# Optimization experiments

Measured on AMD Instinct MI355X. Metric: run time of the kernel, lower is better.

The kernel has to match this reference:

```python
import jax, jax.numpy as jnp
import numpy as np

NUM_HEADS = 16
MODEL_DIM = 1024
DEPTH = MODEL_DIM // NUM_HEADS
B, S = 4, 1024


def setup_inputs() -> dict:
    key = jax.random.key(0)
    ks = jax.random.split(key, 12)
    sc = 1.0 / np.sqrt(MODEL_DIM)
    q = jax.random.normal(ks[0], (B, S, MODEL_DIM), jnp.float32)
    k = jax.random.normal(ks[1], (B, S, MODEL_DIM), jnp.float32)
    v = jax.random.normal(ks[2], (B, S, MODEL_DIM), jnp.float32)
    # binary padding mask, 1 = masked position (added as mask * -1e9)
    mask = (jax.random.uniform(ks[3], (B, 1, 1, S)) < 0.1).astype(jnp.float32)
    Wq = jax.random.normal(ks[4], (MODEL_DIM, MODEL_DIM), jnp.float32) * sc
    bq = jnp.zeros((MODEL_DIM,), jnp.float32)
    Wk = jax.random.normal(ks[5], (MODEL_DIM, MODEL_DIM), jnp.float32) * sc
    bk = jnp.zeros((MODEL_DIM,), jnp.float32)
    Wv = jax.random.normal(ks[6], (MODEL_DIM, MODEL_DIM), jnp.float32) * sc
    bv = jnp.zeros((MODEL_DIM,), jnp.float32)
    Wo = jax.random.normal(ks[7], (MODEL_DIM, MODEL_DIM), jnp.float32) * sc
    bo = jnp.zeros((MODEL_DIM,), jnp.float32)
    return dict(q=q, k=k, v=v, mask=mask, Wq=Wq, bq=bq, Wk=Wk, bk=bk,
                Wv=Wv, bv=bv, Wo=Wo, bo=bo)


def _split_head(x):
    b, s, _ = x.shape
    return x.reshape(b, s, NUM_HEADS, DEPTH).transpose(0, 2, 1, 3)


def reference(q, k, v, mask, Wq, bq, Wk, bk, Wv, bv, Wo, bo):
    Q = _split_head(q @ Wq + bq)   # (B,H,S,depth)
    K = _split_head(k @ Wk + bk)
    V = _split_head(v @ Wv + bv)
    # NOTE: original divides by k_dim (depth), NOT sqrt(depth) -- keep faithful
    logits = jnp.einsum('bhqd,bhkd->bhqk', Q, K) / jnp.float32(DEPTH)
    logits = logits + mask * (-1e9)
    attn = jax.nn.softmax(logits, axis=-1)         # (B,H,Sq,Sk)
    ctx = jnp.einsum('bhqk,bhkd->bhqd', attn, V)   # (B,H,S,depth)
    ctx = ctx.transpose(0, 2, 1, 3).reshape(q.shape[0], -1, MODEL_DIM)
    out = ctx @ Wo + bo
    return out, attn
```

## Files before the change

### kernel.cpp

```cpp
#include <hip/hip_runtime.h>
#include <stdint.h>
#include <stddef.h>

#define DEV __device__ __forceinline__

typedef __bf16 bf16_t;
typedef bf16_t bf16x8 __attribute__((ext_vector_type(8)));
typedef float f32x4 __attribute__((ext_vector_type(4)));
typedef unsigned short us4 __attribute__((ext_vector_type(4)));
typedef unsigned short us8 __attribute__((ext_vector_type(8)));

DEV float bf2f(unsigned short u) {
    union { unsigned int i; float f; } w; w.i = ((unsigned int)u) << 16; return w.f;
}
DEV unsigned short f2bf(float f) {
    union { unsigned int i; float f; } w; w.f = f;
    unsigned int u = w.i;
    return (unsigned short)((u + 0x7fffu + ((u >> 16) & 1u)) >> 16);
}

DEV void gl_lds16(const void* g, void* l) {
    __builtin_amdgcn_global_load_lds((const __attribute__((address_space(1))) void*)g,
                                     (__attribute__((address_space(3))) void*)l,
                                     16, 0, 0);
}

__global__ void __launch_bounds__(256)
cvt_f32_bf16(const float* __restrict__ src, unsigned short* __restrict__ dst) {
    int idx = (blockIdx.x * 256 + threadIdx.x) * 4;
    f32x4 v = *(const f32x4*)&src[idx];
    us4 o;
#pragma unroll
    for (int i = 0; i < 4; i++) o[i] = f2bf(v[i]);
    *(us4*)&dst[idx] = o;
}

__global__ void __launch_bounds__(256)
transpose_w(const float* __restrict__ W0, const float* __restrict__ W1,
            const float* __restrict__ W2, const float* __restrict__ W3,
            unsigned short* __restrict__ T0, unsigned short* __restrict__ T1,
            unsigned short* __restrict__ T2, unsigned short* __restrict__ T3) {
    const float* W    = (blockIdx.z == 0) ? W0 : (blockIdx.z == 1) ? W1 : (blockIdx.z == 2) ? W2 : W3;
    unsigned short* T = (blockIdx.z == 0) ? T0 : (blockIdx.z == 1) ? T1 : (blockIdx.z == 2) ? T2 : T3;
    __shared__ float t[32][33];
    int tx = threadIdx.x, ty = threadIdx.y;
    int k0 = blockIdx.x * 32, n0 = blockIdx.y * 32;
#pragma unroll
    for (int r = 0; r < 4; r++)
        t[ty + r * 8][tx] = W[(size_t)(k0 + ty + r * 8) * 1024 + n0 + tx];
    __syncthreads();
#pragma unroll
    for (int r = 0; r < 4; r++)
        T[(size_t)(n0 + ty + r * 8) * 1024 + k0 + tx] = f2bf(t[tx][ty + r * 8]);
}

template <int MODE>
__global__ void __launch_bounds__(256)
gemm_bt_128(const unsigned short* __restrict__ A,
            const unsigned short* __restrict__ Bt,
            const float* __restrict__ bias,
            void* __restrict__ CoutV) {
    const int K = 1024;
    __shared__ __align__(16) unsigned short As[128 * 32];
    __shared__ __align__(16) unsigned short Bs[128 * 32];
    int tid = threadIdx.x, lane = tid & 63, wid = tid >> 6;
    int mBase = blockIdx.x * 128, nBase = blockIdx.y * 128;
    int wm = (wid >> 1) * 64, wn = (wid & 1) * 64;
    int c0 = lane & 15, quad = lane >> 4;

    f32x4 acc[4][4] = {};

    for (int k0 = 0; k0 < K; k0 += 32) {
        __syncthreads();
#pragma unroll
        for (int i = 0; i < 2; i++) {
            int cb = wid * 64 + 256 * i;
            int cc = cb + lane;
            int row = cc >> 2, kc = cc & 3;
            gl_lds16(A  + (size_t)(mBase + row) * K + k0 + kc * 8, &As[cb * 8]);
            gl_lds16(Bt + (size_t)(nBase + row) * K + k0 + kc * 8, &Bs[cb * 8]);
        }
        __syncthreads();
        bf16x8 af[4], bfr[4];
#pragma unroll
        for (int t = 0; t < 4; t++) {
            af[t]  = *(const bf16x8*)&As[(wm + t * 16 + c0) * 32 + quad * 8];
            bfr[t] = *(const bf16x8*)&Bs[(wn + t * 16 + c0) * 32 + quad * 8];
        }
#pragma unroll
        for (int mt = 0; mt < 4; mt++)
#pragma unroll
            for (int nt = 0; nt < 4; nt++)
                acc[mt][nt] = __builtin_amdgcn_mfma_f32_16x16x32_bf16(af[mt], bfr[nt], acc[mt][nt], 0, 0, 0);
    }

#pragma unroll
    for (int mt = 0; mt < 4; mt++) {
#pragma unroll
        for (int nt = 0; nt < 4; nt++) {
            int n = nBase + wn + nt * 16 + c0;
            float bv = bias[n];
            if (MODE == 2) {
                unsigned short* Cout = (unsigned short*)CoutV;
                int m0 = mBase + wm + mt * 16 + quad * 4;
                int b = m0 >> 10, s = m0 & 1023, h = n >> 6, d = n & 63;
                us4 pk;
#pragma unroll
                for (int r = 0; r < 4; r++) pk[r] = f2bf(acc[mt][nt][r] + bv);
                *(us4*)&Cout[((size_t)((b * 16 + h) * 64 + d)) * 1024 + s] = pk;
            } else {
#pragma unroll
                for (int r = 0; r < 4; r++) {
                    int m = mBase + wm + mt * 16 + quad * 4 + r;
                    float v = acc[mt][nt][r] + bv;
                    if (MODE == 0) {
                        unsigned short* Cout = (unsigned short*)CoutV;
                        int b = m >> 10, s = m & 1023, h = n >> 6, d = n & 63;
                        Cout[((size_t)((b * 16 + h) * 1024 + s)) * 64 + d] = f2bf(v);
                    } else {
                        float* Cout = (float*)CoutV;
                        Cout[(size_t)m * 1024 + n] = v;
                    }
                }
            }
        }
    }
}

__global__ void __launch_bounds__(256)
attn_softmax(const unsigned short* __restrict__ Qws,
             const unsigned short* __restrict__ Kws,
             const float* __restrict__ maskp,
             float* __restrict__ attnOut) {
    __shared__ __align__(16) unsigned short Ks[256 * 64];
    __shared__ float redbuf[4][16];

    int tid = threadIdx.x, lane = tid & 63, wid = tid >> 6;
    int c0 = lane & 15, quad = lane >> 4;
    int bh = blockIdx.y, b = bh >> 4;
    int q0 = blockIdx.x * 16;

    bf16x8 aq0, aq1;
    {
        const unsigned short* qp = Qws + ((size_t)bh * 1024 + q0 + c0) * 64 + quad * 8;
        aq0 = *(const bf16x8*)qp;
        aq1 = *(const bf16x8*)(qp + 32);
    }

    f32x4 acc[16] = {};

    for (int ch = 0; ch < 4; ch++) {
        __syncthreads();
#pragma unroll
        for (int i = 0; i < 8; i++) {
            int cb = wid * 64 + 256 * i;
            int cc = cb + lane;
            int row = cc >> 3, kc = cc & 7;
            gl_lds16(Kws + ((size_t)bh * 1024 + ch * 256 + row) * 64 + kc * 8, &Ks[cb * 8]);
        }
        __syncthreads();
#pragma unroll
        for (int nt = 0; nt < 4; nt++) {
            int srow = wid * 64 + nt * 16 + c0;
            const unsigned short* kp = &Ks[srow * 64 + quad * 8];
            bf16x8 b0 = *(const bf16x8*)kp;
            bf16x8 b1 = *(const bf16x8*)(kp + 32);
            int ai = ch * 4 + nt;
            acc[ai] = __builtin_amdgcn_mfma_f32_16x16x32_bf16(aq0, b0, acc[ai], 0, 0, 0);
            acc[ai] = __builtin_amdgcn_mfma_f32_16x16x32_bf16(aq1, b1, acc[ai], 0, 0, 0);
        }
    }

    float lmax[4] = {-3e38f, -3e38f, -3e38f, -3e38f};
#pragma unroll
    for (int i = 0; i < 16; i++) {
        int col = (i >> 2) * 256 + wid * 64 + (i & 3) * 16 + c0;
        float mval = maskp[b * 1024 + col] * (-1e9f);
#pragma unroll
        for (int r = 0; r < 4; r++) {
            float v = acc[i][r] * (1.0f / 64.0f) + mval;
            acc[i][r] = v;
            lmax[r] = fmaxf(lmax[r], v);
        }
    }
#pragma unroll
    for (int st = 1; st < 16; st <<= 1) {
#pragma unroll
        for (int r = 0; r < 4; r++) lmax[r] = fmaxf(lmax[r], __shfl_xor(lmax[r], st, 64));
    }
    if (c0 == 0) {
#pragma unroll
        for (int r = 0; r < 4; r++) redbuf[wid][quad * 4 + r] = lmax[r];
    }
    __syncthreads();
    float rmax[4];
#pragma unroll
    for (int r = 0; r < 4; r++) {
        int row = quad * 4 + r;
        rmax[r] = fmaxf(fmaxf(redbuf[0][row], redbuf[1][row]), fmaxf(redbuf[2][row], redbuf[3][row]));
    }
    float lsum[4] = {0.f, 0.f, 0.f, 0.f};
#pragma unroll
    for (int i = 0; i < 16; i++) {
#pragma unroll
        for (int r = 0; r < 4; r++) {
            float e = __expf(acc[i][r] - rmax[r]);
            acc[i][r] = e;
            lsum[r] += e;
        }
    }
#pragma unroll
    for (int st = 1; st < 16; st <<= 1) {
#pragma unroll
        for (int r = 0; r < 4; r++) lsum[r] += __shfl_xor(lsum[r], st, 64);
    }
    __syncthreads();
    if (c0 == 0) {
#pragma unroll
        for (int r = 0; r < 4; r++) redbuf[wid][quad * 4 + r] = lsum[r];
    }
    __syncthreads();
    float rinv[4];
#pragma unroll
    for (int r = 0; r < 4; r++) {
        int row = quad * 4 + r;
        rinv[r] = 1.0f / (redbuf[0][row] + redbuf[1][row] + redbuf[2][row] + redbuf[3][row]);
    }
    size_t base = ((size_t)bh * 1024 + q0) * 1024;
#pragma unroll
    for (int i = 0; i < 16; i++) {
        int col = (i >> 2) * 256 + wid * 64 + (i & 3) * 16 + c0;
#pragma unroll
        for (int r = 0; r < 4; r++) {
            int row = quad * 4 + r;
            attnOut[base + (size_t)row * 1024 + col] = acc[i][r] * rinv[r];
        }
    }
}

__global__ void __launch_bounds__(256)
pv_gemm(const float* __restrict__ attn,
        const unsigned short* __restrict__ Vt,
        unsigned short* __restrict__ ctx) {
    __shared__ __align__(16) float Asf[128 * 64];
    __shared__ __align__(16) unsigned short Bs[64 * 64];
    int tid = threadIdx.x, lane = tid & 63, wid = tid >> 6;
    int c0 = lane & 15, quad = lane >> 4;
    int bh = blockIdx.y, b = bh >> 4, h = bh & 15;
    int mBase = blockIdx.x * 128;
    const float* Ab = attn + (size_t)bh * 1024 * 1024;
    const unsigned short* Bb = Vt + (size_t)bh * 64 * 1024;

    f32x4 acc[2][4] = {};

    for (int k0 = 0; k0 < 1024; k0 += 64) {
        __syncthreads();
#pragma unroll
        for (int i = 0; i < 8; i++) {
            int cb = wid * 64 + 256 * i;
            int cc = cb + lane;
            int row = cc >> 4, kc = cc & 15;
            gl_lds16(Ab + (size_t)(mBase + row) * 1024 + k0 + kc * 4, &Asf[cb * 4]);
        }
#pragma unroll
        for (int i = 0; i < 2; i++) {
            int cb = wid * 64 + 256 * i;
            int cc = cb + lane;
            int row = cc >> 3, kc = cc & 7;
            gl_lds16(Bb + (size_t)row * 1024 + k0 + kc * 8, &Bs[cb * 8]);
        }
        __syncthreads();
#pragma unroll
        for (int ks = 0; ks < 2; ks++) {
            bf16x8 af[2], bfr[4];
#pragma unroll
            for (int mt = 0; mt < 2; mt++) {
                const float* ap = &Asf[(wid * 32 + mt * 16 + c0) * 64 + ks * 32 + quad * 8];
                union { us8 u; bf16x8 b; } cv;
#pragma unroll
                for (int j = 0; j < 8; j++) cv.u[j] = f2bf(ap[j]);
                af[mt] = cv.b;
            }
#pragma unroll
            for (int nt = 0; nt < 4; nt++)
                bfr[nt] = *(const bf16x8*)&Bs[(nt * 16 + c0) * 64 + ks * 32 + quad * 8];
#pragma unroll
            for (int mt = 0; mt < 2; mt++)
#pragma unroll
                for (int nt = 0; nt < 4; nt++)
                    acc[mt][nt] = __builtin_amdgcn_mfma_f32_16x16x32_bf16(af[mt], bfr[nt], acc[mt][nt], 0, 0, 0);
        }
    }
#pragma unroll
    for (int mt = 0; mt < 2; mt++)
#pragma unroll
        for (int nt = 0; nt < 4; nt++)
#pragma unroll
            for (int r = 0; r < 4; r++) {
                int s = mBase + wid * 32 + mt * 16 + quad * 4 + r;
                int d = nt * 16 + c0;
                ctx[((size_t)(b * 1024 + s)) * 1024 + h * 64 + d] = f2bf(acc[mt][nt][r]);
            }
}

extern "C" void kernel_launch(void* const* d_in, const int* in_sizes, int n_in,
                              void* d_out, int out_size, void* d_ws, size_t ws_size,
                              hipStream_t stream) {
    (void)in_sizes; (void)n_in; (void)out_size; (void)ws_size;
    const float* q    = (const float*)d_in[0];
    const float* k    = (const float*)d_in[1];
    const float* v    = (const float*)d_in[2];
    const float* mask = (const float*)d_in[3];
    const float* Wq   = (const float*)d_in[4];
    const float* bq   = (const float*)d_in[5];
    const float* Wk   = (const float*)d_in[6];
    const float* bk   = (const float*)d_in[7];
    const float* Wv   = (const float*)d_in[8];
    const float* bv   = (const float*)d_in[9];
    const float* Wo   = (const float*)d_in[10];
    const float* bo   = (const float*)d_in[11];

    float* outF  = (float*)d_out;
    float* attnF = outF + (size_t)4 * 1024 * 1024;

    unsigned short* wsu = (unsigned short*)d_ws;
    const size_t M1 = (size_t)1024 * 1024;
    unsigned short* WqT = wsu;
    unsigned short* WkT = wsu + 1 * M1;
    unsigned short* WvT = wsu + 2 * M1;
    unsigned short* WoT = wsu + 3 * M1;
    unsigned short* tmp = wsu + 4 * M1;
    unsigned short* Qw  = wsu + 8 * M1;
    unsigned short* Kw  = wsu + 12 * M1;
    unsigned short* Vtw = wsu + 16 * M1;
    unsigned short* ctx = wsu + 20 * M1;

    transpose_w<<<dim3(32, 32, 4), dim3(32, 8), 0, stream>>>(Wq, Wk, Wv, Wo, WqT, WkT, WvT, WoT);

    cvt_f32_bf16<<<4096, 256, 0, stream>>>(q, tmp);
    gemm_bt_128<0><<<dim3(32, 8), 256, 0, stream>>>(tmp, WqT, bq, Qw);
    cvt_f32_bf16<<<4096, 256, 0, stream>>>(k, tmp);
    gemm_bt_128<0><<<dim3(32, 8), 256, 0, stream>>>(tmp, WkT, bk, Kw);
    cvt_f32_bf16<<<4096, 256, 0, stream>>>(v, tmp);
    gemm_bt_128<2><<<dim3(32, 8), 256, 0, stream>>>(tmp, WvT, bv, Vtw);

    attn_softmax<<<dim3(64, 64), 256, 0, stream>>>(Qw, Kw, mask, attnF);

    pv_gemm<<<dim3(8, 64), 256, 0, stream>>>(attnF, Vtw, ctx);

    gemm_bt_128<1><<<dim3(32, 8), 256, 0, stream>>>(ctx, WoT, bo, outF);
}
```

Baseline: 533.5 us.

## Fuse PV matmul into softmax kernel and batch QKV conversions and GEMMs

The P·V product now runs inside the attention-softmax kernel: normalized probabilities are written to global memory for the attn output and also stored as bf16 in swizzled LDS, then multiplied against V tiles loaded from the transposed V workspace. This removes the separate pv_gemm kernel, which re-read the full fp32 attention matrix from HBM. The three input conversions and the three QKV projection GEMMs are each merged into a single launch using blockIdx.z, which cuts launch count and fills more CUs per launch. In exchange LDS use per block rises to about 70KB, which may lower occupancy of the attention kernel, and the workspace grows to hold separate q/k/v bf16 buffers.

```diff
diff --git a/kernel.cpp b/kernel.cpp
--- a/kernel.cpp
+++ b/kernel.cpp
@@ -26,7 +26,10 @@
 }
 
 __global__ void __launch_bounds__(256)
-cvt_f32_bf16(const float* __restrict__ src, unsigned short* __restrict__ dst) {
+cvt3(const float* __restrict__ s0, const float* __restrict__ s1, const float* __restrict__ s2,
+     unsigned short* __restrict__ d0, unsigned short* __restrict__ d1, unsigned short* __restrict__ d2) {
+    const float* src    = (blockIdx.z == 0) ? s0 : (blockIdx.z == 1) ? s1 : s2;
+    unsigned short* dst = (blockIdx.z == 0) ? d0 : (blockIdx.z == 1) ? d1 : d2;
     int idx = (blockIdx.x * 256 + threadIdx.x) * 4;
     f32x4 v = *(const f32x4*)&src[idx];
     us4 o;
@@ -54,12 +57,85 @@
         T[(size_t)(n0 + ty + r * 8) * 1024 + k0 + tx] = f2bf(t[tx][ty + r * 8]);
 }
 
-template <int MODE>
-__global__ void __launch_bounds__(256)
-gemm_bt_128(const unsigned short* __restrict__ A,
-            const unsigned short* __restrict__ Bt,
-            const float* __restrict__ bias,
-            void* __restrict__ CoutV) {
+__global__ void __launch_bounds__(256)
+qkv_gemm(const unsigned short* __restrict__ Aq, const unsigned short* __restrict__ Ak,
+         const unsigned short* __restrict__ Av,
+         const unsigned short* __restrict__ BtQ, const unsigned short* __restrict__ BtK,
+         const unsigned short* __restrict__ BtV,
+         const float* __restrict__ biq, const float* __restrict__ bik,
+         const float* __restrict__ biv,
+         unsigned short* __restrict__ Qw, unsigned short* __restrict__ Kw,
+         unsigned short* __restrict__ Vtw) {
+    const int K = 1024;
+    const unsigned short* A  = (blockIdx.z == 0) ? Aq  : (blockIdx.z == 1) ? Ak  : Av;
+    const unsigned short* Bt = (blockIdx.z == 0) ? BtQ : (blockIdx.z == 1) ? BtK : BtV;
+    const float* bias        = (blockIdx.z == 0) ? biq : (blockIdx.z == 1) ? bik : biv;
+    unsigned short* Cout     = (blockIdx.z == 0) ? Qw  : (blockIdx.z == 1) ? Kw  : Vtw;
+    const bool vmode = (blockIdx.z == 2);
+
+    __shared__ __align__(16) unsigned short As[128 * 32];
+    __shared__ __align__(16) unsigned short Bs[128 * 32];
+    int tid = threadIdx.x, lane = tid & 63, wid = tid >> 6;
+    int mBase = blockIdx.x * 128, nBase = blockIdx.y * 128;
+    int wm = (wid >> 1) * 64, wn = (wid & 1) * 64;
+    int c0 = lane & 15, quad = lane >> 4;
+
+    f32x4 acc[4][4] = {};
+
+    for (int k0 = 0; k0 < K; k0 += 32) {
+        __syncthreads();
+#pragma unroll
+        for (int i = 0; i < 2; i++) {
+            int cb = wid * 64 + 256 * i;
+            int cc = cb + lane;
+            int row = cc >> 2, kc = cc & 3;
+            gl_lds16(A  + (size_t)(mBase + row) * K + k0 + kc * 8, &As[cb * 8]);
+            gl_lds16(Bt + (size_t)(nBase + row) * K + k0 + kc * 8, &Bs[cb * 8]);
+        }
+        __syncthreads();
+        bf16x8 af[4], bfr[4];
+#pragma unroll
+        for (int t = 0; t < 4; t++) {
+            af[t]  = *(const bf16x8*)&As[(wm + t * 16 + c0) * 32 + quad * 8];
+            bfr[t] = *(const bf16x8*)&Bs[(wn + t * 16 + c0) * 32 + quad * 8];
+        }
+#pragma unroll
+        for (int mt = 0; mt < 4; mt++)
+#pragma unroll
+            for (int nt = 0; nt < 4; nt++)
+                acc[mt][nt] = __builtin_amdgcn_mfma_f32_16x16x32_bf16(af[mt], bfr[nt], acc[mt][nt], 0, 0, 0);
+    }
+
+#pragma unroll
+    for (int mt = 0; mt < 4; mt++) {
+#pragma unroll
+        for (int nt = 0; nt < 4; nt++) {
+            int n = nBase + wn + nt * 16 + c0;
+            float bv = bias[n];
+            if (vmode) {
+                int m0 = mBase + wm + mt * 16 + quad * 4;
+                int b = m0 >> 10, s = m0 & 1023, h = n >> 6, d = n & 63;
+                us4 pk;
+#pragma unroll
+                for (int r = 0; r < 4; r++) pk[r] = f2bf(acc[mt][nt][r] + bv);
+                *(us4*)&Cout[((size_t)((b * 16 + h) * 64 + d)) * 1024 + s] = pk;
+            } else {
+#pragma unroll
+                for (int r = 0; r < 4; r++) {
+                    int m = mBase + wm + mt * 16 + quad * 4 + r;
+                    int b = m >> 10, s = m & 1023, h = n >> 6, d = n & 63;
+                    Cout[((size_t)((b * 16 + h) * 1024 + s)) * 64 + d] = f2bf(acc[mt][nt][r] + bv);
+                }
+            }
+        }
+    }
+}
+
+__global__ void __launch_bounds__(256)
+out_gemm(const unsigned short* __restrict__ A,
+         const unsigned short* __restrict__ Bt,
+         const float* __restrict__ bias,
+         float* __restrict__ Cout) {
     const int K = 1024;
     __shared__ __align__(16) unsigned short As[128 * 32];
     __shared__ __align__(16) unsigned short Bs[128 * 32];
@@ -93,51 +169,34 @@
             for (int nt = 0; nt < 4; nt++)
                 acc[mt][nt] = __builtin_amdgcn_mfma_f32_16x16x32_bf16(af[mt], bfr[nt], acc[mt][nt], 0, 0, 0);
     }
-
-#pragma unroll
-    for (int mt = 0; mt < 4; mt++) {
+#pragma unroll
+    for (int mt = 0; mt < 4; mt++)
 #pragma unroll
         for (int nt = 0; nt < 4; nt++) {
             int n = nBase + wn + nt * 16 + c0;
             float bv = bias[n];
-            if (MODE == 2) {
-                unsigned short* Cout = (unsigned short*)CoutV;
-                int m0 = mBase + wm + mt * 16 + quad * 4;
-                int b = m0 >> 10, s = m0 & 1023, h = n >> 6, d = n & 63;
-                us4 pk;
-#pragma unroll
-                for (int r = 0; r < 4; r++) pk[r] = f2bf(acc[mt][nt][r] + bv);
-                *(us4*)&Cout[((size_t)((b * 16 + h) * 64 + d)) * 1024 + s] = pk;
-            } else {
-#pragma unroll
-                for (int r = 0; r < 4; r++) {
-                    int m = mBase + wm + mt * 16 + quad * 4 + r;
-                    float v = acc[mt][nt][r] + bv;
-                    if (MODE == 0) {
-                        unsigned short* Cout = (unsigned short*)CoutV;
-                        int b = m >> 10, s = m & 1023, h = n >> 6, d = n & 63;
-                        Cout[((size_t)((b * 16 + h) * 1024 + s)) * 64 + d] = f2bf(v);
-                    } else {
-                        float* Cout = (float*)CoutV;
-                        Cout[(size_t)m * 1024 + n] = v;
-                    }
-                }
+#pragma unroll
+            for (int r = 0; r < 4; r++) {
+                int m = mBase + wm + mt * 16 + quad * 4 + r;
+                Cout[(size_t)m * 1024 + n] = acc[mt][nt][r] + bv;
             }
         }
-    }
-}
-
-__global__ void __launch_bounds__(256)
-attn_softmax(const unsigned short* __restrict__ Qws,
-             const unsigned short* __restrict__ Kws,
-             const float* __restrict__ maskp,
-             float* __restrict__ attnOut) {
-    __shared__ __align__(16) unsigned short Ks[256 * 64];
+}
+
+__global__ void __launch_bounds__(256)
+attn_pv(const unsigned short* __restrict__ Qws,
+        const unsigned short* __restrict__ Kws,
+        const unsigned short* __restrict__ Vtw,
+        const float* __restrict__ maskp,
+        float* __restrict__ attnOut,
+        unsigned short* __restrict__ ctx) {
+    __shared__ __align__(16) unsigned short ldsA[17408];
+    __shared__ __align__(16) unsigned short Vs[17408];
     __shared__ float redbuf[4][16];
 
     int tid = threadIdx.x, lane = tid & 63, wid = tid >> 6;
     int c0 = lane & 15, quad = lane >> 4;
-    int bh = blockIdx.y, b = bh >> 4;
+    int bh = blockIdx.y, b = bh >> 4, h = bh & 15;
     int q0 = blockIdx.x * 16;
 
     bf16x8 aq0, aq1;
@@ -156,13 +215,13 @@
             int cb = wid * 64 + 256 * i;
             int cc = cb + lane;
             int row = cc >> 3, kc = cc & 7;
-            gl_lds16(Kws + ((size_t)bh * 1024 + ch * 256 + row) * 64 + kc * 8, &Ks[cb * 8]);
+            gl_lds16(Kws + ((size_t)bh * 1024 + ch * 256 + row) * 64 + kc * 8, &ldsA[cb * 8]);
         }
         __syncthreads();
 #pragma unroll
         for (int nt = 0; nt < 4; nt++) {
             int srow = wid * 64 + nt * 16 + c0;
-            const unsigned short* kp = &Ks[srow * 64 + quad * 8];
+            const unsigned short* kp = &ldsA[srow * 64 + quad * 8];
             bf16x8 b0 = *(const bf16x8*)kp;
             bf16x8 b1 = *(const bf16x8*)(kp + 32);
             int ai = ch * 4 + nt;
@@ -226,81 +285,50 @@
         int row = quad * 4 + r;
         rinv[r] = 1.0f / (redbuf[0][row] + redbuf[1][row] + redbuf[2][row] + redbuf[3][row]);
     }
-    size_t base = ((size_t)bh * 1024 + q0) * 1024;
+
+    size_t gbase = ((size_t)bh * 1024 + q0) * 1024;
 #pragma unroll
     for (int i = 0; i < 16; i++) {
+        int kk = (i >> 2) * 64 + (i & 3) * 16 + c0;
         int col = (i >> 2) * 256 + wid * 64 + (i & 3) * 16 + c0;
+        int kks = kk ^ (quad << 3);
 #pragma unroll
         for (int r = 0; r < 4; r++) {
             int row = quad * 4 + r;
-            attnOut[base + (size_t)row * 1024 + col] = acc[i][r] * rinv[r];
-        }
-    }
-}
-
-__global__ void __launch_bounds__(256)
-pv_gemm(const float* __restrict__ attn,
-        const unsigned short* __restrict__ Vt,
-        unsigned short* __restrict__ ctx) {
-    __shared__ __align__(16) float Asf[128 * 64];
-    __shared__ __align__(16) unsigned short Bs[64 * 64];
-    int tid = threadIdx.x, lane = tid & 63, wid = tid >> 6;
-    int c0 = lane & 15, quad = lane >> 4;
-    int bh = blockIdx.y, b = bh >> 4, h = bh & 15;
-    int mBase = blockIdx.x * 128;
-    const float* Ab = attn + (size_t)bh * 1024 * 1024;
-    const unsigned short* Bb = Vt + (size_t)bh * 64 * 1024;
-
-    f32x4 acc[2][4] = {};
-
-    for (int k0 = 0; k0 < 1024; k0 += 64) {
+            float pv = acc[i][r] * rinv[r];
+            attnOut[gbase + (size_t)row * 1024 + col] = pv;
+            ldsA[wid * 4352 + row * 272 + kks] = f2bf(pv);
+        }
+    }
+
+    f32x4 ctxacc = {};
+    for (int ch = 0; ch < 4; ch++) {
         __syncthreads();
 #pragma unroll
         for (int i = 0; i < 8; i++) {
-            int cb = wid * 64 + 256 * i;
-            int cc = cb + lane;
-            int row = cc >> 4, kc = cc & 15;
-            gl_lds16(Ab + (size_t)(mBase + row) * 1024 + k0 + kc * 4, &Asf[cb * 4]);
-        }
-#pragma unroll
-        for (int i = 0; i < 2; i++) {
-            int cb = wid * 64 + 256 * i;
-            int cc = cb + lane;
-            int row = cc >> 3, kc = cc & 7;
-            gl_lds16(Bb + (size_t)row * 1024 + k0 + kc * 8, &Bs[cb * 8]);
-        }
-        __syncthreads();
-#pragma unroll
-        for (int ks = 0; ks < 2; ks++) {
-            bf16x8 af[2], bfr[4];
-#pragma unroll
-            for (int mt = 0; mt < 2; mt++) {
-                const float* ap = &Asf[(wid * 32 + mt * 16 + c0) * 64 + ks * 32 + quad * 8];
-                union { us8 u; bf16x8 b; } cv;
-#pragma unroll
-                for (int j = 0; j < 8; j++) cv.u[j] = f2bf(ap[j]);
-                af[mt] = cv.b;
+            int cidx = tid + 256 * i;
+            int drow = cidx >> 5;
+            int soff = (cidx & 31) * 8;
+            us8 val = *(const us8*)&Vtw[((size_t)(bh * 64 + drow)) * 1024 + ch * 256 + soff];
+            *(us8*)&Vs[drow * 272 + soff] = val;
+        }
+        __syncthreads();
+#pragma unroll
+        for (int wv = 0; wv < 4; wv++) {
+#pragma unroll
+            for (int t = 0; t < 2; t++) {
+                int kidx = (ch * 64 + t * 32 + quad * 8) ^ ((c0 >> 2) << 3);
+                bf16x8 a  = *(const bf16x8*)&ldsA[wv * 4352 + c0 * 272 + kidx];
+                bf16x8 bf_ = *(const bf16x8*)&Vs[(wid * 16 + c0) * 272 + wv * 64 + t * 32 + quad * 8];
+                ctxacc = __builtin_amdgcn_mfma_f32_16x16x32_bf16(a, bf_, ctxacc, 0, 0, 0);
             }
-#pragma unroll
-            for (int nt = 0; nt < 4; nt++)
-                bfr[nt] = *(const bf16x8*)&Bs[(nt * 16 + c0) * 64 + ks * 32 + quad * 8];
-#pragma unroll
-            for (int mt = 0; mt < 2; mt++)
-#pragma unroll
-                for (int nt = 0; nt < 4; nt++)
-                    acc[mt][nt] = __builtin_amdgcn_mfma_f32_16x16x32_bf16(af[mt], bfr[nt], acc[mt][nt], 0, 0, 0);
-        }
-    }
-#pragma unroll
-    for (int mt = 0; mt < 2; mt++)
-#pragma unroll
-        for (int nt = 0; nt < 4; nt++)
-#pragma unroll
-            for (int r = 0; r < 4; r++) {
-                int s = mBase + wid * 32 + mt * 16 + quad * 4 + r;
-                int d = nt * 16 + c0;
-                ctx[((size_t)(b * 1024 + s)) * 1024 + h * 64 + d] = f2bf(acc[mt][nt][r]);
-            }
+        }
+    }
+#pragma unroll
+    for (int r = 0; r < 4; r++) {
+        int s = q0 + quad * 4 + r;
+        ctx[((size_t)(b * 1024 + s)) * 1024 + h * 64 + wid * 16 + c0] = f2bf(ctxacc[r]);
+    }
 }
 
 extern "C" void kernel_launch(void* const* d_in, const int* in_sizes, int n_in,
@@ -325,28 +353,25 @@
 
     unsigned short* wsu = (unsigned short*)d_ws;
     const size_t M1 = (size_t)1024 * 1024;
-    unsigned short* WqT = wsu;
+    unsigned short* WqT = wsu + 0 * M1;
     unsigned short* WkT = wsu + 1 * M1;
     unsigned short* WvT = wsu + 2 * M1;
     unsigned short* WoT = wsu + 3 * M1;
-    unsigned short* tmp = wsu + 4 * M1;
-    unsigned short* Qw  = wsu + 8 * M1;
-    unsigned short* Kw  = wsu + 12 * M1;
-    unsigned short* Vtw = wsu + 16 * M1;
-    unsigned short* ctx = wsu + 20 * M1;
+    unsigned short* tq  = wsu + 4 * M1;
+    unsigned short* tk  = wsu + 8 * M1;
+    unsigned short* tv  = wsu + 12 * M1;
+    unsigned short* Qw  = wsu + 16 * M1;
+    unsigned short* Kw  = wsu + 20 * M1;
+    unsigned short* Vtw = wsu + 24 * M1;
+    unsigned short* ctx = wsu + 28 * M1;
 
     transpose_w<<<dim3(32, 32, 4), dim3(32, 8), 0, stream>>>(Wq, Wk, Wv, Wo, WqT, WkT, WvT, WoT);
 
-    cvt_f32_bf16<<<4096, 256, 0, stream>>>(q, tmp);
-    gemm_bt_128<0><<<dim3(32, 8), 256, 0, stream>>>(tmp, WqT, bq, Qw);
-    cvt_f32_bf16<<<4096, 256, 0, stream>>>(k, tmp);
-    gemm_bt_128<0><<<dim3(32, 8), 256, 0, stream>>>(tmp, WkT, bk, Kw);
-    cvt_f32_bf16<<<4096, 256, 0, stream>>>(v, tmp);
-    gemm_bt_128<2><<<dim3(32, 8), 256, 0, stream>>>(tmp, WvT, bv, Vtw);
-
-    attn_softmax<<<dim3(64, 64), 256, 0, stream>>>(Qw, Kw, mask, attnF);
-
-    pv_gemm<<<dim3(8, 64), 256, 0, stream>>>(attnF, Vtw, ctx);
-
-    gemm_bt_128<1><<<dim3(32, 8), 256, 0, stream>>>(ctx, WoT, bo, outF);
-}
+    cvt3<<<dim3(4096, 1, 3), 256, 0, stream>>>(q, k, v, tq, tk, tv);
+
+    qkv_gemm<<<dim3(32, 8, 3), 256, 0, stream>>>(tq, tk, tv, WqT, WkT, WvT, bq, bk, bv, Qw, Kw, Vtw);
+
+    attn_pv<<<dim3(64, 64), 256, 0, stream>>>(Qw, Kw, Vtw, mask, attnF, ctx);
+
+    out_gemm<<<dim3(32, 8), 256, 0, stream>>>(ctx, WoT, bo, outF);
+}
```

Measured after the change: 493.7 us. -7.4%, faster.
